# Kernel optimization log

Hardware: AMD Instinct MI355X
Metric: run time of the kernel (lower is better)

Reference implementation:

```python
import jax, jax.numpy as jnp
import numpy as np

GAMMA = 1.0
LAMBDA = 0.5
CLAMP = (-10.0, 10.0)


def setup_inputs() -> dict:
    key = jax.random.key(0)
    k1, k2, k3 = jax.random.split(key, 3)
    m, S, D = 64, 4096, 128
    generated_samples = jax.random.normal(k1, (m, S, D), dtype=jnp.float32)
    target_sample = jax.random.normal(k2, (S, D), dtype=jnp.float32)
    time_points = jax.random.uniform(k3, (S,), dtype=jnp.float32)
    return {
        "generated_samples": generated_samples,
        "target_sample": target_sample,
        "time_points": time_points,
    }


def reference(generated_samples, target_sample, time_points):
    # paths = concat([time, values], -1); since time_points is shared across all
    # paths, the time column cancels in path_i - path_j, so the RBF kernel
    # k(x,y)=exp(-gamma*||x-y||^2) depends only on the value tensors.
    m = generated_samples.shape[0]
    X = generated_samples.reshape(m, -1)          # [m, S*D]
    t = target_sample.reshape(-1)                 # [S*D]

    # Pairwise squared distances via gram trick (one pass over X, tiny GEMM).
    sq = jnp.sum(X * X, axis=1)                   # [m]
    gram = X @ X.T                                # [m, m]
    d2 = jnp.maximum(sq[:, None] + sq[None, :] - 2.0 * gram, 0.0)
    K = jnp.exp(-GAMMA * d2)                      # [m, m]
    # off-diagonal sum (diag of K is exp(0)=1 -> subtract m)
    cross_sum = jnp.sum(K) - jnp.trace(K)
    cross_term = (LAMBDA / 2.0) * cross_sum / (m * (m - 1))

    # E[k(X, Y)] against target
    dt2 = jnp.sum((X - t[None, :]) ** 2, axis=1)  # [m]
    target_term = jnp.mean(jnp.exp(-GAMMA * dt2))

    score = cross_term - target_term
    return jnp.clip(score, CLAMP[0], CLAMP[1])
```

## Files before the change

### kernel.cpp

```cpp
#include <hip/hip_runtime.h>
#include <hip/hip_bf16.h>

#define NROW 65
#define GP   80
#define GE   (GP * GP)
#define CHF  32
#define ROWB 128
#define NRB  66
#define BUFB (NRB * ROWB)
#define WBUF (2 * BUFB)
#define TPB  256
#define GRID_MAX 512

typedef float  f32x4  __attribute__((ext_vector_type(4)));
typedef __bf16 bf16x8 __attribute__((ext_vector_type(8)));

__device__ __forceinline__ void gl_lds16(const void* g, void* l) {
  __builtin_amdgcn_global_load_lds(
      (const __attribute__((address_space(1))) void*)g,
      (__attribute__((address_space(3))) void*)l, 16, 0, 0);
}

__global__ __launch_bounds__(TPB) void gram_k(
    const float* __restrict__ X,
    const float* __restrict__ T,
    float* __restrict__ S,
    int Nk, int nch)
{
  __shared__ __align__(16) char smem[4 * WBUF];
  const int tid  = threadIdx.x;
  const int wv   = tid >> 6;
  const int lane = tid & 63;
  const int lr   = lane & 15, kg = lane >> 4;
  const size_t Nkb = (size_t)Nk * 4;

  char* myb = smem + wv * WBUF;

  f32x4 acc[15];
#pragma unroll
  for (int i = 0; i < 15; ++i) acc[i] = (f32x4){0.f, 0.f, 0.f, 0.f};

  auto stage = [&](char* buf, int c) {
    const size_t colb = (size_t)c * ROWB;
#pragma unroll
    for (int i = 0; i < 8; ++i) {
      const int r  = 8 * i + (lane >> 3);
      const int ss = (lane & 7) ^ ((lane >> 3) & 7);
      const char* src = (const char*)X + (size_t)r * Nkb + colb + ss * 16;
      gl_lds16(src, buf + i * 1024);
    }
    if (lane < 8) {
      const char* src = (const char*)T + colb + lane * 16;
      gl_lds16(src, buf + 64 * ROWB);
    }
  };

  const int nwaves = gridDim.x * (TPB / 64);
  int c = blockIdx.x * (TPB / 64) + wv;
  stage(myb, c);
  int it = 0;
  while (true) {
    char* cur = myb + (it & 1) * BUFB;
    char* nxt = myb + ((it & 1) ^ 1) * BUFB;
    const int cn = c + nwaves;
    const bool hn = cn < nch;
    asm volatile("s_waitcnt lgkmcnt(0)" ::: "memory");
    __builtin_amdgcn_sched_barrier(0);
    if (hn) stage(nxt, cn);
    if (hn) asm volatile("s_waitcnt vmcnt(9)" ::: "memory");
    else    asm volatile("s_waitcnt vmcnt(0)" ::: "memory");
    __builtin_amdgcn_sched_barrier(0);

    bf16x8 f[5];
#pragma unroll
    for (int t = 0; t < 5; ++t) {
      int r = t * 16 + lr; if (r > 65) r = 65;
      const char* rb = cur + r * ROWB;
      const int sw = (r & 7) << 4;
      f32x4 a = *(const f32x4*)(rb + ((kg * 32) ^ sw));
      f32x4 b = *(const f32x4*)(rb + ((kg * 32 + 16) ^ sw));
      f[t] = (bf16x8){(__bf16)a.x, (__bf16)a.y, (__bf16)a.z, (__bf16)a.w,
                      (__bf16)b.x, (__bf16)b.y, (__bf16)b.z, (__bf16)b.w};
    }
#pragma unroll
    for (int I = 0; I < 5; ++I)
#pragma unroll
      for (int J = I; J < 5; ++J) {
        const int idx = I * 5 + J - (I * (I + 1)) / 2;
        acc[idx] = __builtin_amdgcn_mfma_f32_16x16x32_bf16(f[I], f[J], acc[idx], 0, 0, 0);
      }
    if (!hn) break;
    c = cn; ++it;
  }

  float* gl = (float*)smem;
  __syncthreads();
  for (int e = tid; e < GE; e += TPB) gl[e] = 0.f;
  __syncthreads();
  for (int w = 0; w < 4; ++w) {
    if (wv == w) {
#pragma unroll
      for (int I = 0; I < 5; ++I)
#pragma unroll
        for (int J = I; J < 5; ++J) {
          const int idx = I * 5 + J - (I * (I + 1)) / 2;
#pragma unroll
          for (int r = 0; r < 4; ++r) {
            const int grow = I * 16 + kg * 4 + r;
            const int gcol = J * 16 + lr;
            gl[grow * GP + gcol] += acc[idx][r];
          }
        }
    }
    __syncthreads();
  }
  float* dst = S + (size_t)blockIdx.x * GE;
  for (int e = tid; e < GE; e += TPB) dst[e] = gl[e];
}

#define RBLK 64
__global__ __launch_bounds__(256) void reduce_k(
    const float* __restrict__ S, float* __restrict__ G, int nsl)
{
  __shared__ float ps[4][RBLK];
  const int tid = threadIdx.x;
  const int e0  = blockIdx.x * RBLK;
  const int el  = tid & (RBLK - 1);
  const int p   = tid >> 6;
  const float* base = S + (size_t)p * GE + (e0 + el);
  float s = 0.f;
  int i = p;
#pragma unroll 8
  for (; i + 32 <= nsl; i += 32) {
    s += base[0];
    s += base[(size_t)4  * GE];
    s += base[(size_t)8  * GE];
    s += base[(size_t)12 * GE];
    s += base[(size_t)16 * GE];
    s += base[(size_t)20 * GE];
    s += base[(size_t)24 * GE];
    s += base[(size_t)28 * GE];
    base += (size_t)32 * GE;
  }
  for (; i < nsl; i += 4) { s += base[0]; base += (size_t)4 * GE; }
  ps[p][el] = s;
  __syncthreads();
  if (tid < RBLK)
    G[e0 + tid] = ps[0][tid] + ps[1][tid] + ps[2][tid] + ps[3][tid];
}

__global__ __launch_bounds__(256) void epilogue_k(
    const float* __restrict__ G, float* __restrict__ out)
{
  __shared__ float gl[GE];
  __shared__ float rx[4], rt[4];
  const int tid = threadIdx.x;
  for (int e = tid; e < GE; e += 256) gl[e] = G[e];
  __syncthreads();

  float accX = 0.f, accT = 0.f;
  for (int e = tid; e < GE; e += 256) {
    int i = e / GP, j = e % GP;
    if (j >= NROW || i >= j) continue;
    float g  = gl[e];
    float d2 = gl[i * GP + i] + gl[j * GP + j] - 2.f * g;
    if (j < 64) accX += expf(-fmaxf(d2, 0.f));
    else        accT += expf(-d2);
  }
#pragma unroll
  for (int off = 32; off > 0; off >>= 1) {
    accX += __shfl_down(accX, off);
    accT += __shfl_down(accT, off);
  }
  const int wv = tid >> 6, lane = tid & 63;
  if (lane == 0) { rx[wv] = accX; rt[wv] = accT; }
  __syncthreads();
  if (tid == 0) {
    float sx = rx[0] + rx[1] + rx[2] + rx[3];
    float st = rt[0] + rt[1] + rt[2] + rt[3];
    float score = sx / 8064.f - st / 64.f;
    score = fminf(fmaxf(score, -10.f), 10.f);
    out[0] = score;
  }
}

extern "C" void kernel_launch(void* const* d_in, const int* in_sizes, int n_in,
                              void* d_out, int out_size, void* d_ws, size_t ws_size,
                              hipStream_t stream) {
  const float* X = (const float*)d_in[0];
  const float* T = (const float*)d_in[1];
  float* out = (float*)d_out;

  const int Nk  = in_sizes[1];
  const int nch = Nk / CHF;

  int nsl = (int)(ws_size / (GE * sizeof(float))) - 1;
  if (nsl > GRID_MAX) nsl = GRID_MAX;
  if (nsl < 1) nsl = 1;
  float* S = (float*)d_ws;
  float* G = S + (size_t)nsl * GE;

  gram_k<<<nsl, TPB, 0, stream>>>(X, T, S, Nk, nch);
  reduce_k<<<(GE / RBLK), 256, 0, stream>>>(S, G, nsl);
  epilogue_k<<<1, 256, 0, stream>>>(G, out);
}
```

Baseline: 210.0 us.

## Pre-pack inputs to chunk-interleaved bf16 layout before the Gram MFMA pass

Adds a pack kernel that converts X and the target to bf16 and stores them chunk-major, with all 65 rows of each 64-column chunk contiguous. The Gram kernel then loads its MFMA fragments straight from global memory, dropping the LDS double-buffering, the swizzle and the in-loop fp32-to-bf16 conversion. The aim is cheaper, more contiguous loads in the hot loop with no conversion work there. The cost is an extra full pass that reads the fp32 input and writes a bf16 copy, and the hot loop now has no explicit prefetch. The pack launch grid is hardcoded for this problem shape.

New measurement: 233.8 us. 1.11x slower.

```diff
diff --git a/kernel.cpp b/kernel.cpp
--- a/kernel.cpp
+++ b/kernel.cpp
@@ -4,97 +4,74 @@
 #define NROW 65
 #define GP   80
 #define GE   (GP * GP)
-#define CHF  32
-#define ROWB 128
-#define NRB  66
-#define BUFB (NRB * ROWB)
-#define WBUF (2 * BUFB)
+#define C2F  64
+#define CROW 66
+#define CELEM (CROW * C2F)
 #define TPB  256
-#define GRID_MAX 512
+#define GRID_B 512
 
 typedef float  f32x4  __attribute__((ext_vector_type(4)));
 typedef __bf16 bf16x8 __attribute__((ext_vector_type(8)));
 
-__device__ __forceinline__ void gl_lds16(const void* g, void* l) {
-  __builtin_amdgcn_global_load_lds(
-      (const __attribute__((address_space(1))) void*)g,
-      (__attribute__((address_space(3))) void*)l, 16, 0, 0);
+__global__ __launch_bounds__(TPB) void pack_k(
+    const float* __restrict__ X, const float* __restrict__ T,
+    __bf16* __restrict__ P, int Nk)
+{
+  const int job   = blockIdx.x;
+  const int row   = job >> 8;
+  const int strip = job & 255;
+  const int tid   = threadIdx.x;
+  const int c2    = strip * 32 + (tid >> 3);
+  const int klo   = (tid & 7) * 8;
+
+  const float* src = ((row < 64) ? (X + (size_t)row * Nk) : T)
+                     + (size_t)c2 * C2F + klo;
+  f32x4 a = *(const f32x4*)src;
+  f32x4 b = *(const f32x4*)(src + 4);
+  bf16x8 h = (bf16x8){(__bf16)a.x, (__bf16)a.y, (__bf16)a.z, (__bf16)a.w,
+                      (__bf16)b.x, (__bf16)b.y, (__bf16)b.z, (__bf16)b.w};
+  *(bf16x8*)(P + (size_t)c2 * CELEM + row * C2F + klo) = h;
 }
 
-__global__ __launch_bounds__(TPB) void gram_k(
-    const float* __restrict__ X,
-    const float* __restrict__ T,
+__global__ __launch_bounds__(TPB) void gram_b(
+    const __bf16* __restrict__ P,
     float* __restrict__ S,
-    int Nk, int nch)
+    int nc2)
 {
-  __shared__ __align__(16) char smem[4 * WBUF];
+  __shared__ float gl[GE];
   const int tid  = threadIdx.x;
   const int wv   = tid >> 6;
   const int lane = tid & 63;
   const int lr   = lane & 15, kg = lane >> 4;
-  const size_t Nkb = (size_t)Nk * 4;
-
-  char* myb = smem + wv * WBUF;
 
   f32x4 acc[15];
 #pragma unroll
   for (int i = 0; i < 15; ++i) acc[i] = (f32x4){0.f, 0.f, 0.f, 0.f};
 
-  auto stage = [&](char* buf, int c) {
-    const size_t colb = (size_t)c * ROWB;
+  const int nw = gridDim.x * (TPB / 64);
+  const int gw = blockIdx.x * (TPB / 64) + wv;
+
+  for (int c2 = gw; c2 < nc2; c2 += nw) {
+    const __bf16* base = P + (size_t)c2 * CELEM;
+    bf16x8 f[2][5];
 #pragma unroll
-    for (int i = 0; i < 8; ++i) {
-      const int r  = 8 * i + (lane >> 3);
-      const int ss = (lane & 7) ^ ((lane >> 3) & 7);
-      const char* src = (const char*)X + (size_t)r * Nkb + colb + ss * 16;
-      gl_lds16(src, buf + i * 1024);
-    }
-    if (lane < 8) {
-      const char* src = (const char*)T + colb + lane * 16;
-      gl_lds16(src, buf + 64 * ROWB);
-    }
-  };
-
-  const int nwaves = gridDim.x * (TPB / 64);
-  int c = blockIdx.x * (TPB / 64) + wv;
-  stage(myb, c);
-  int it = 0;
-  while (true) {
-    char* cur = myb + (it & 1) * BUFB;
-    char* nxt = myb + ((it & 1) ^ 1) * BUFB;
-    const int cn = c + nwaves;
-    const bool hn = cn < nch;
-    asm volatile("s_waitcnt lgkmcnt(0)" ::: "memory");
-    __builtin_amdgcn_sched_barrier(0);
-    if (hn) stage(nxt, cn);
-    if (hn) asm volatile("s_waitcnt vmcnt(9)" ::: "memory");
-    else    asm volatile("s_waitcnt vmcnt(0)" ::: "memory");
-    __builtin_amdgcn_sched_barrier(0);
-
-    bf16x8 f[5];
+    for (int s = 0; s < 2; ++s)
 #pragma unroll
-    for (int t = 0; t < 5; ++t) {
-      int r = t * 16 + lr; if (r > 65) r = 65;
-      const char* rb = cur + r * ROWB;
-      const int sw = (r & 7) << 4;
-      f32x4 a = *(const f32x4*)(rb + ((kg * 32) ^ sw));
-      f32x4 b = *(const f32x4*)(rb + ((kg * 32 + 16) ^ sw));
-      f[t] = (bf16x8){(__bf16)a.x, (__bf16)a.y, (__bf16)a.z, (__bf16)a.w,
-                      (__bf16)b.x, (__bf16)b.y, (__bf16)b.z, (__bf16)b.w};
-    }
+      for (int t = 0; t < 5; ++t) {
+        int r = t * 16 + lr; if (r > 65) r = 65;
+        f[s][t] = *(const bf16x8*)(base + r * C2F + s * 32 + kg * 8);
+      }
 #pragma unroll
-    for (int I = 0; I < 5; ++I)
+    for (int s = 0; s < 2; ++s)
 #pragma unroll
-      for (int J = I; J < 5; ++J) {
-        const int idx = I * 5 + J - (I * (I + 1)) / 2;
-        acc[idx] = __builtin_amdgcn_mfma_f32_16x16x32_bf16(f[I], f[J], acc[idx], 0, 0, 0);
-      }
-    if (!hn) break;
-    c = cn; ++it;
+      for (int I = 0; I < 5; ++I)
+#pragma unroll
+        for (int J = I; J < 5; ++J) {
+          const int idx = I * 5 + J - (I * (I + 1)) / 2;
+          acc[idx] = __builtin_amdgcn_mfma_f32_16x16x32_bf16(f[s][I], f[s][J], acc[idx], 0, 0, 0);
+        }
   }
 
-  float* gl = (float*)smem;
-  __syncthreads();
   for (int e = tid; e < GE; e += TPB) gl[e] = 0.f;
   __syncthreads();
   for (int w = 0; w < 4; ++w) {
@@ -192,15 +169,20 @@
   float* out = (float*)d_out;
 
   const int Nk  = in_sizes[1];
-  const int nch = Nk / CHF;
+  const int nc2 = Nk / C2F;
 
-  int nsl = (int)(ws_size / (GE * sizeof(float))) - 1;
-  if (nsl > GRID_MAX) nsl = GRID_MAX;
+  size_t p_bytes = (size_t)nc2 * CELEM * sizeof(__bf16);
+  p_bytes = (p_bytes + 255) & ~(size_t)255;
+  __bf16* P = (__bf16*)d_ws;
+  size_t rem = (ws_size > p_bytes) ? (ws_size - p_bytes) : 0;
+  int nsl = (int)(rem / (GE * sizeof(float))) - 1;
+  if (nsl > GRID_B) nsl = GRID_B;
   if (nsl < 1) nsl = 1;
-  float* S = (float*)d_ws;
+  float* S = (float*)((char*)d_ws + p_bytes);
   float* G = S + (size_t)nsl * GE;
 
-  gram_k<<<nsl, TPB, 0, stream>>>(X, T, S, Nk, nch);
+  pack_k<<<65 * 256, TPB, 0, stream>>>(X, T, P, Nk);
+  gram_b<<<nsl, TPB, 0, stream>>>(P, S, nc2);
   reduce_k<<<(GE / RBLK), 256, 0, stream>>>(S, G, nsl);
   epilogue_k<<<1, 256, 0, stream>>>(G, out);
 }
```
